# Kernel optimization log

Measured on AMD Instinct MI355X. Metric: run time of the kernel, lower is better.

## Reference

```python
import jax, jax.numpy as jnp
import numpy as np

H, W = 64, 64          # self.shape = (W, H) = (64, 64)
REG_MAX = 16
TOPK = 4

def _dwconv(y, w, b):
    # y: (N, L, C) -> depthwise 3x3 conv on (N, C, H, W) -> (N, L, C)
    N, L, C = y.shape
    img = jnp.transpose(y, (0, 2, 1)).reshape(N, C, H, W)
    out = jax.lax.conv_general_dilated(
        img, w, (1, 1), ((1, 1), (1, 1)),
        dimension_numbers=('NCHW', 'OIHW', 'NCHW'), feature_group_count=C)
    out = out + b[None, :, None, None]
    return jnp.transpose(out.reshape(N, C, H * W), (0, 2, 1))

def _mlp(x, fc1_w, fc1_b, dw1_w, dw1_b, fc2_w, fc2_b, dw2_w, dw2_b, fc3_w, fc3_b):
    h = x @ fc1_w.T + fc1_b
    h = jax.nn.gelu(_dwconv(h, dw1_w, dw1_b), approximate=False)  # torch nn.GELU is exact erf
    h = h @ fc2_w.T + fc2_b
    h = jax.nn.gelu(_dwconv(h, dw2_w, dw2_b), approximate=False)
    return h @ fc3_w.T + fc3_b

def setup_inputs() -> dict:
    key = jax.random.key(0)
    ks = iter(jax.random.split(key, 16))
    d = {}
    d['x'] = jax.random.normal(next(ks), (1, 32, H * W, 256), dtype=jnp.float32)
    for p in ('c_', 'r_'):
        out3 = 1 if p == 'c_' else 4 * (REG_MAX + 1)
        d[p + 'fc1_w'] = 0.02 * jax.random.normal(next(ks), (256, 256), dtype=jnp.float32)
        d[p + 'fc1_b'] = jnp.zeros((256,), jnp.float32)
        d[p + 'dw1_w'] = 0.3 * jax.random.normal(next(ks), (256, 1, 3, 3), dtype=jnp.float32)
        d[p + 'dw1_b'] = jnp.zeros((256,), jnp.float32)
        d[p + 'fc2_w'] = 0.02 * jax.random.normal(next(ks), (256, 256), dtype=jnp.float32)
        d[p + 'fc2_b'] = jnp.zeros((256,), jnp.float32)
        d[p + 'dw2_w'] = 0.3 * jax.random.normal(next(ks), (256, 1, 3, 3), dtype=jnp.float32)
        d[p + 'dw2_b'] = jnp.zeros((256,), jnp.float32)
        d[p + 'fc3_w'] = 0.02 * jax.random.normal(next(ks), (out3, 256), dtype=jnp.float32)
        d[p + 'fc3_b'] = jnp.zeros((out3,), jnp.float32)
    d['rc1_w'] = 0.1 * jax.random.normal(next(ks), (64, 4 * (TOPK + 1)), dtype=jnp.float32)
    d['rc1_b'] = jnp.zeros((64,), jnp.float32)
    d['rc2_w'] = 0.1 * jax.random.normal(next(ks), (1, 64), dtype=jnp.float32)
    d['rc2_b'] = jnp.zeros((1,), jnp.float32)
    return d

def reference(x,
              c_fc1_w, c_fc1_b, c_dw1_w, c_dw1_b, c_fc2_w, c_fc2_b, c_dw2_w, c_dw2_b, c_fc3_w, c_fc3_b,
              r_fc1_w, r_fc1_b, r_dw1_w, r_dw1_b, r_fc2_w, r_fc2_b, r_dw2_w, r_dw2_b, r_fc3_w, r_fc3_b,
              rc1_w, rc1_b, rc2_w, rc2_b):
    xs = x[0]                                   # (N, L, C)
    N = xs.shape[0]
    reg_pred = _mlp(xs, r_fc1_w, r_fc1_b, r_dw1_w, r_dw1_b, r_fc2_w, r_fc2_b,
                    r_dw2_w, r_dw2_b, r_fc3_w, r_fc3_b)  # (N, L, 4*(reg_max+1))
    prob = jax.nn.softmax(
        jnp.transpose(reg_pred, (0, 2, 1)).reshape(N, 4, REG_MAX + 1, H, W), axis=2)
    pt = jnp.transpose(prob, (0, 1, 3, 4, 2))   # (N,4,H,W,reg_max+1)
    topk, _ = jax.lax.top_k(pt, TOPK)           # (N,4,H,W,topk), sorted desc like torch
    stat = jnp.concatenate([topk, topk.mean(axis=-1, keepdims=True)], axis=-1)
    stat = jnp.transpose(stat, (0, 1, 4, 2, 3)).reshape(N, 4 * (TOPK + 1), H, W)
    q = jax.nn.relu(jnp.einsum('nchw,oc->nohw', stat, rc1_w) + rc1_b[None, :, None, None])
    q = jax.nn.sigmoid(jnp.einsum('nchw,oc->nohw', q, rc2_w) + rc2_b[None, :, None, None])
    cls = _mlp(xs, c_fc1_w, c_fc1_b, c_dw1_w, c_dw1_b, c_fc2_w, c_fc2_b,
               c_dw2_w, c_dw2_b, c_fc3_w, c_fc3_b)      # (N, L, 1)
    cls = jax.nn.sigmoid(jnp.transpose(cls, (0, 2, 1)).reshape(N, 1, H, W)) * q
    proj = jnp.arange(REG_MAX + 1, dtype=reg_pred.dtype)  # linspace(0, reg_max, reg_max+1)
    dist = jax.nn.softmax(reg_pred.reshape(-1, REG_MAX + 1), axis=1) @ proj
    boxes = dist.reshape(N, H, W, 4) / REG_MAX
    return cls, boxes, reg_pred.reshape(N, H, W, 4 * (REG_MAX + 1))
```

## Files before the change

### kernel.cpp

```cpp
#include <hip/hip_runtime.h>
#include <hip/hip_bf16.h>

typedef __bf16 bf16x8 __attribute__((ext_vector_type(8)));
typedef float f32x4 __attribute__((ext_vector_type(4)));
typedef float f32x2 __attribute__((ext_vector_type(2)));

__device__ __forceinline__ float bf2f(unsigned short b) {
  unsigned int u = ((unsigned int)b) << 16;
  return __builtin_bit_cast(float, u);
}
__device__ __forceinline__ unsigned short f2bf(float f) {
  unsigned int u = __builtin_bit_cast(unsigned int, f);
  unsigned int r = u + 0x7fffu + ((u >> 16) & 1u);
  return (unsigned short)(r >> 16);
}
__device__ __forceinline__ f32x2 unpack2(unsigned int u) {
  f32x2 r;
  r.x = __builtin_bit_cast(float, u << 16);
  r.y = __builtin_bit_cast(float, u & 0xffff0000u);
  return r;
}

__device__ __forceinline__ void gload16(const void* g, void* l) {
  typedef __attribute__((address_space(1))) const void* gp_t;
  typedef __attribute__((address_space(3))) void* lp_t;
  __builtin_amdgcn_global_load_lds((gp_t)g, (lp_t)l, 16, 0, 0);
}

__device__ __forceinline__ f32x2 gelu2(f32x2 x) {
  f32x2 m = x * x;
  f32x2 t = m * (-0.10295273f) + (-2.3021967f);
  f32x2 u = x * t;
  f32x2 e;
  e.x = __builtin_amdgcn_exp2f(u.x);
  e.y = __builtin_amdgcn_exp2f(u.y);
  f32x2 d = e + 1.0f;
  f32x2 r;
  r.x = __builtin_amdgcn_rcpf(d.x);
  r.y = __builtin_amdgcn_rcpf(d.y);
  return x * r;
}
__device__ __forceinline__ unsigned int cvt_pk_bf16(float lo, float hi) {
  unsigned int r;
  asm("v_cvt_pk_bf16_f32 %0, %1, %2" : "=v"(r) : "v"(lo), "v"(hi));
  return r;
}

__global__ __launch_bounds__(256) void prep_all(
    const float* __restrict__ c1w, const float* __restrict__ r1w,
    const float* __restrict__ c2w, const float* __restrict__ r2w,
    const float* __restrict__ c3w, const float* __restrict__ r3w, const float* __restrict__ r3b,
    const float* __restrict__ c1b, const float* __restrict__ r1b,
    const float* __restrict__ c2b, const float* __restrict__ r2b,
    const float* __restrict__ d1wc, const float* __restrict__ d1bc,
    const float* __restrict__ d1wr, const float* __restrict__ d1br,
    const float* __restrict__ d2wc, const float* __restrict__ d2bc,
    const float* __restrict__ d2wr, const float* __restrict__ d2br,
    unsigned short* __restrict__ w1cat, unsigned short* __restrict__ w2cat,
    unsigned short* __restrict__ c3wb, unsigned short* __restrict__ wr3pad,
    float* __restrict__ br3pad, float* __restrict__ b1cat, float* __restrict__ b2cat,
    float* __restrict__ wd1, float* __restrict__ bd1,
    float* __restrict__ wd2, float* __restrict__ bd2) {
  int i = blockIdx.x * 256 + threadIdx.x;
  {
    int which = i >> 16, j = i & 65535;
    float v = (which == 0) ? c1w[j] : (which == 1) ? r1w[j] : (which == 2) ? c2w[j] : r2w[j];
    unsigned short* dst = (which < 2) ? (w1cat + which * 65536) : (w2cat + (which - 2) * 65536);
    dst[j] = f2bf(v);
  }
  if (i < 32768) {
    int r = i >> 8, c = i & 255;
    wr3pad[i] = (r < 68) ? f2bf(r3w[r * 256 + c]) : (unsigned short)0;
    if (i < 128) br3pad[i] = (i < 68) ? r3b[i] : 0.f;
  }
  if (i < 256) c3wb[i] = f2bf(c3w[i]);
  if (i < 4608) {
    int tap = i >> 9, ch = i & 511, cc = ch & 255;
    wd1[i] = (ch < 256) ? d1wc[cc * 9 + tap] : d1wr[cc * 9 + tap];
    wd2[i] = (ch < 256) ? d2wc[cc * 9 + tap] : d2wr[cc * 9 + tap];
  }
  if (i < 512) {
    bd1[i] = (i < 256) ? d1bc[i] : d1br[i & 255];
    bd2[i] = (i < 256) ? d2bc[i] : d2br[i & 255];
    b1cat[i] = (i < 256) ? c1b[i] : r1b[i & 255];
    b2cat[i] = (i < 256) ? c2b[i] : r2b[i & 255];
  }
}

__global__ __launch_bounds__(256, 2) void gemm_f32a(
    const float* __restrict__ X,
    const unsigned short* __restrict__ W,
    const float* __restrict__ bias,
    unsigned short* __restrict__ Out, int ldo, int lnN) {
  __shared__ unsigned short ldsA[32768];
  __shared__ unsigned short ldsB[2][4096];
  const int nwg = gridDim.x;
  const int bid = blockIdx.x;
  const int wg = (bid & 7) * (nwg >> 3) + (bid >> 3);
  const int mtile = wg >> lnN;
  const int ntile = wg & ((1 << lnN) - 1);
  const long row0 = (long)mtile * 128;
  const int col0 = ntile * 128;

  const int tid = threadIdx.x;
  const int lane = tid & 63;
  const int wid = tid >> 6;
  const int wr = (wid >> 1) * 64;
  const int wc = (wid & 1) * 64;
  const int rr = lane & 15;
  const int gk = lane >> 4;
  const int swz = (rr >> 1) & 3;

  const int srow_l = (wid << 4) + (lane >> 2);
  const int sgl = lane & 3;

  #pragma unroll 4
  for (int j = 0; j < 16; j++) {
    const int s = j * 256 + tid;
    const int row = s >> 5;
    const int glog = s & 31;
    const float* src = X + (row0 + row) * 256L + glog * 8;
    const float4 v0 = *(const float4*)(src);
    const float4 v1 = *(const float4*)(src + 4);
    uint4 pk;
    pk.x = cvt_pk_bf16(v0.x, v0.y);
    pk.y = cvt_pk_bf16(v0.z, v0.w);
    pk.z = cvt_pk_bf16(v1.x, v1.y);
    pk.w = cvt_pk_bf16(v1.z, v1.w);
    const int phys = glog ^ (row & 7);
    *(uint4*)&ldsA[(row * 32 + phys) * 8] = pk;
  }

  auto stageB = [&](int buf, int k0) {
    #pragma unroll
    for (int j = 0; j < 2; j++) {
      const int slotbase = j * 256 + (wid << 6);
      const int row = j * 64 + srow_l;
      const int g = sgl ^ ((row >> 1) & 3);
      gload16(W + (long)(col0 + row) * 256 + k0 + g * 8,
              &ldsB[buf][slotbase * 8]);
    }
  };

  f32x4 acc[4][4] = {};
  stageB(0, 0);
  asm volatile("s_waitcnt vmcnt(0) lgkmcnt(0)" ::: "memory");
  __builtin_amdgcn_s_barrier();

  #pragma unroll
  for (int ks = 0; ks < 8; ks++) {
    if (ks < 7) {
      stageB((ks + 1) & 1, (ks + 1) * 32);
      asm volatile("s_waitcnt vmcnt(2)" ::: "memory");
    } else {
      asm volatile("s_waitcnt vmcnt(0)" ::: "memory");
    }
    __builtin_amdgcn_s_barrier();
    asm volatile("" ::: "memory");
    const unsigned short* bufB = ldsB[ks & 1];
    bf16x8 af[4], bf[4];
    #pragma unroll
    for (int mi = 0; mi < 4; mi++) {
      const int arow = wr + mi * 16 + rr;
      const int aphys = (ks * 4 + gk) ^ (arow & 7);
      af[mi] = __builtin_bit_cast(bf16x8,
          *(const uint4*)&ldsA[(arow * 32 + aphys) * 8]);
    }
    #pragma unroll
    for (int ni = 0; ni < 4; ni++)
      bf[ni] = __builtin_bit_cast(bf16x8,
          *(const uint4*)&bufB[((wc + ni * 16 + rr) * 4 + (gk ^ swz)) * 8]);
    #pragma unroll
    for (int mi = 0; mi < 4; mi++)
      #pragma unroll
      for (int ni = 0; ni < 4; ni++)
        acc[mi][ni] = __builtin_amdgcn_mfma_f32_16x16x32_bf16(af[mi], bf[ni], acc[mi][ni], 0, 0, 0);
    asm volatile("" ::: "memory");
    __builtin_amdgcn_s_barrier();
  }

  #pragma unroll
  for (int mi = 0; mi < 4; mi++) {
    const int rbase = wr + mi * 16 + (lane >> 4) * 4;
    #pragma unroll
    for (int ni = 0; ni < 4; ni++) {
      const int c_ = wc + ni * 16 + (lane & 15);
      const float bv = bias[col0 + c_];
      #pragma unroll
      for (int r = 0; r < 4; r++) {
        Out[(row0 + rbase + r) * (long)ldo + col0 + c_] = f2bf(acc[mi][ni][r] + bv);
      }
    }
  }
}

__global__ __launch_bounds__(256, 3) void gemm_glds(
    const unsigned short* __restrict__ A, int lda, int zAoff,
    const unsigned short* __restrict__ W, int zWoff,
    const float* __restrict__ bias, int zBoff,
    unsigned short* __restrict__ Out, int ldo, int zOoff, int lnN,
    float* __restrict__ OutF) {
  __shared__ unsigned short lds[2][8192];
  const int z = blockIdx.z;
  const unsigned short* Az = A + (long)z * zAoff;
  const unsigned short* Wz = W + (long)z * zWoff;
  const float* biasz = bias + z * zBoff;
  unsigned short* Outz = Out + (long)z * zOoff;

  const int nwg = gridDim.x;
  const int bid = blockIdx.x;
  const int wg = (bid & 7) * (nwg >> 3) + (bid >> 3);
  const int mtile = wg >> lnN;
  const int ntile = wg & ((1 << lnN) - 1);
  const long row0 = (long)mtile * 128;
  const int col0 = ntile * 128;

  const int tid = threadIdx.x;
  const int lane = tid & 63;
  const int wid = tid >> 6;
  const int wr = (wid >> 1) * 64;
  const int wc = (wid & 1) * 64;
  const int rr = lane & 15;
  const int gk = lane >> 4;
  const int swz = (rr >> 1) & 3;

  const int srow_l = (wid << 4) + (lane >> 2);
  const int sgl = lane & 3;

  f32x4 acc[4][4] = {};

  auto stage = [&](int buf, int k0) {
    #pragma unroll
    for (int j = 0; j < 4; j++) {
      const int slotbase = j * 256 + (wid << 6);
      unsigned short* ldst = &lds[buf][slotbase * 8];
      const int row = (j & 1) * 64 + srow_l;
      const int g = sgl ^ ((row >> 1) & 3);
      const unsigned short* src;
      if (j < 2) src = Az + (row0 + row) * (long)lda + k0 + g * 8;
      else       src = Wz + (long)(col0 + row) * 256 + k0 + g * 8;
      gload16(src, ldst);
    }
  };

  stage(0, 0);
  #pragma unroll
  for (int ks = 0; ks < 8; ks++) {
    if (ks < 7) {
      stage((ks + 1) & 1, (ks + 1) * 32);
      asm volatile("s_waitcnt vmcnt(4)" ::: "memory");
    } else {
      asm volatile("s_waitcnt vmcnt(0)" ::: "memory");
    }
    __builtin_amdgcn_s_barrier();
    asm volatile("" ::: "memory");
    const unsigned short* buf = lds[ks & 1];
    bf16x8 af[4], bf[4];
    #pragma unroll
    for (int mi = 0; mi < 4; mi++)
      af[mi] = __builtin_bit_cast(bf16x8,
          *(const uint4*)&buf[(wr + mi * 16 + rr) * 32 + ((gk ^ swz) * 8)]);
    #pragma unroll
    for (int ni = 0; ni < 4; ni++)
      bf[ni] = __builtin_bit_cast(bf16x8,
          *(const uint4*)&buf[4096 + (wc + ni * 16 + rr) * 32 + ((gk ^ swz) * 8)]);
    #pragma unroll
    for (int mi = 0; mi < 4; mi++)
      #pragma unroll
      for (int ni = 0; ni < 4; ni++)
        acc[mi][ni] = __builtin_amdgcn_mfma_f32_16x16x32_bf16(af[mi], bf[ni], acc[mi][ni], 0, 0, 0);
    asm volatile("" ::: "memory");
    __builtin_amdgcn_s_barrier();
  }

  #pragma unroll
  for (int mi = 0; mi < 4; mi++) {
    const int rbase = wr + mi * 16 + (lane >> 4) * 4;
    #pragma unroll
    for (int ni = 0; ni < 4; ni++) {
      const int c_ = wc + ni * 16 + (lane & 15);
      const float bv = biasz[col0 + c_];
      #pragma unroll
      for (int r = 0; r < 4; r++) {
        const float val = acc[mi][ni][r] + bv;
        Outz[(row0 + rbase + r) * (long)ldo + col0 + c_] = f2bf(val);
        if (OutF != nullptr && c_ < 68)
          OutF[(row0 + rbase + r) * 68L + c_] = val;
      }
    }
  }
}

template <bool CLS>
__global__ __launch_bounds__(256) void dwconv_gelu4(
    const unsigned short* __restrict__ In,
    const float* __restrict__ Wt, const float* __restrict__ Bt,
    unsigned short* __restrict__ Out,
    const unsigned short* __restrict__ Wc3, const float* __restrict__ bc3,
    float* __restrict__ cls_logit) {
  const int t = blockIdx.x * 256 + threadIdx.x;
  const int g = t & 63;
  const int p = t >> 6;
  const int n = p >> 10;
  const int h = (p >> 4) & 63;
  const int w0 = (p & 15) << 2;
  const int cbase = g << 3;
  f32x2 acc[4][4];
  {
    float4 b0 = *(const float4*)(Bt + cbase);
    float4 b1 = *(const float4*)(Bt + cbase + 4);
    f32x2 bb[4];
    bb[0].x = b0.x; bb[0].y = b0.y; bb[1].x = b0.z; bb[1].y = b0.w;
    bb[2].x = b1.x; bb[2].y = b1.y; bb[3].x = b1.z; bb[3].y = b1.w;
    #pragma unroll
    for (int k = 0; k < 4; k++)
      #pragma unroll
      for (int i = 0; i < 4; i++) acc[k][i] = bb[i];
  }
  #pragma unroll
  for (int dy = -1; dy <= 1; dy++) {
    const int hh = h + dy;
    if (hh < 0 || hh > 63) continue;
    const float* wbase = Wt + ((dy + 1) * 3) * 512 + cbase;
    f32x2 wt[3][4];
    #pragma unroll
    for (int j = 0; j < 3; j++) {
      float4 a0 = *(const float4*)(wbase + j * 512);
      float4 a1 = *(const float4*)(wbase + j * 512 + 4);
      wt[j][0].x = a0.x; wt[j][0].y = a0.y; wt[j][1].x = a0.z; wt[j][1].y = a0.w;
      wt[j][2].x = a1.x; wt[j][2].y = a1.y; wt[j][3].x = a1.z; wt[j][3].y = a1.w;
    }
    const long rowtok = (long)(((n << 6) + hh) << 6);
    f32x2 f[6][4];
    #pragma unroll
    for (int d = 0; d < 6; d++) {
      const int col = w0 - 1 + d;
      uint4 v = {0u, 0u, 0u, 0u};
      if (col >= 0 && col < 64)
        v = *(const uint4*)(In + (rowtok + col) * 512 + cbase);
      f[d][0] = unpack2(v.x); f[d][1] = unpack2(v.y);
      f[d][2] = unpack2(v.z); f[d][3] = unpack2(v.w);
    }
    #pragma unroll
    for (int k = 0; k < 4; k++)
      #pragma unroll
      for (int j = 0; j < 3; j++)
        #pragma unroll
        for (int i = 0; i < 4; i++)
          acc[k][i] += f[k + j][i] * wt[j][i];
  }
  f32x2 w3[4];
  if (CLS) {
    const int cc = cbase & 255;
    uint4 wv = *(const uint4*)(Wc3 + cc);
    w3[0] = unpack2(wv.x); w3[1] = unpack2(wv.y);
    w3[2] = unpack2(wv.z); w3[3] = unpack2(wv.w);
  }
  const long mbase = ((long)((n << 6) + h) << 6) + w0;
  float s[4];
  #pragma unroll
  for (int k = 0; k < 4; k++) {
    __align__(16) unsigned int ov[4];
    f32x2 ge[4];
    #pragma unroll
    for (int i = 0; i < 4; i++) {
      ge[i] = gelu2(acc[k][i]);
      ov[i] = cvt_pk_bf16(ge[i].x, ge[i].y);
    }
    if (!CLS || cbase >= 256)
      *(uint4*)(Out + (mbase + k) * 512 + cbase) = *(uint4*)ov;
    if (CLS) {
      f32x2 sp = ge[0] * w3[0] + ge[1] * w3[1] + ge[2] * w3[2] + ge[3] * w3[3];
      s[k] = sp.x + sp.y;
    }
  }
  if (CLS) {
    #pragma unroll
    for (int k = 0; k < 4; k++) {
      #pragma unroll
      for (int m = 16; m >= 1; m >>= 1) s[k] += __shfl_xor(s[k], m);
    }
    if (g == 0) {
      float b = bc3[0];
      float4 o;
      o.x = s[0] + b; o.y = s[1] + b; o.z = s[2] + b; o.w = s[3] + b;
      *(float4*)(cls_logit + mbase) = o;
    }
  }
}

__global__ __launch_bounds__(256) void post_kernel(
    const unsigned short* __restrict__ RP,
    const float* __restrict__ cls_logit,
    const float* __restrict__ rc1_w, const float* __restrict__ rc1_b,
    const float* __restrict__ rc2_w, const float* __restrict__ rc2_b,
    float* __restrict__ out_cls, float* __restrict__ out_boxes) {
  int m = blockIdx.x * 256 + threadIdx.x;
  const unsigned short* rp = RP + (long)m * 128;
  __align__(16) unsigned short raw[72];
  #pragma unroll
  for (int q = 0; q < 9; q++)
    *(uint4*)(raw + q * 8) = *(const uint4*)(rp + q * 8);
  float stat[20];
  float4 boxes;
  #pragma unroll
  for (int s = 0; s < 4; s++) {
    float v[17];
    float mx = -1e30f;
    #pragma unroll
    for (int i = 0; i < 17; i++) {
      v[i] = bf2f(raw[s * 17 + i]);
      mx = fmaxf(mx, v[i]);
    }
    float sum = 0.f;
    #pragma unroll
    for (int i = 0; i < 17; i++) { v[i] = __expf(v[i] - mx); sum += v[i]; }
    float inv = 1.f / sum;
    float dist = 0.f;
    #pragma unroll
    for (int i = 0; i < 17; i++) { v[i] *= inv; dist += v[i] * (float)i; }
    ((float*)&boxes)[s] = dist * 0.0625f;
    float tk[4];
    #pragma unroll
    for (int t = 0; t < 4; t++) {
      float bm = v[0]; int bi = 0;
      #pragma unroll
      for (int i = 1; i < 17; i++) {
        if (v[i] > bm) { bm = v[i]; bi = i; }
      }
      tk[t] = bm;
      #pragma unroll
      for (int i = 0; i < 17; i++)
        if (i == bi) v[i] = -1.f;
    }
    stat[s * 5 + 0] = tk[0]; stat[s * 5 + 1] = tk[1];
    stat[s * 5 + 2] = tk[2]; stat[s * 5 + 3] = tk[3];
    stat[s * 5 + 4] = 0.25f * (tk[0] + tk[1] + tk[2] + tk[3]);
  }
  *(float4*)(out_boxes + (long)m * 4) = boxes;
  float z = 0.f;
  #pragma unroll
  for (int o = 0; o < 64; o++) {
    float q = rc1_b[o];
    #pragma unroll
    for (int c = 0; c < 20; c++) q += rc1_w[o * 20 + c] * stat[c];
    q = fmaxf(q, 0.f);
    z += q * rc2_w[o];
  }
  z += rc2_b[0];
  float q2 = 1.f / (1.f + __expf(-z));
  float cl = 1.f / (1.f + __expf(-cls_logit[m]));
  out_cls[m] = cl * q2;
}

extern "C" void kernel_launch(void* const* d_in, const int* in_sizes, int n_in,
                              void* d_out, int out_size, void* d_ws, size_t ws_size,
                              hipStream_t stream) {
  const float* x       = (const float*)d_in[0];
  const float* c_fc1_w = (const float*)d_in[1];
  const float* c_fc1_b = (const float*)d_in[2];
  const float* c_dw1_w = (const float*)d_in[3];
  const float* c_dw1_b = (const float*)d_in[4];
  const float* c_fc2_w = (const float*)d_in[5];
  const float* c_fc2_b = (const float*)d_in[6];
  const float* c_dw2_w = (const float*)d_in[7];
  const float* c_dw2_b = (const float*)d_in[8];
  const float* c_fc3_w = (const float*)d_in[9];
  const float* c_fc3_b = (const float*)d_in[10];
  const float* r_fc1_w = (const float*)d_in[11];
  const float* r_fc1_b = (const float*)d_in[12];
  const float* r_dw1_w = (const float*)d_in[13];
  const float* r_dw1_b = (const float*)d_in[14];
  const float* r_fc2_w = (const float*)d_in[15];
  const float* r_fc2_b = (const float*)d_in[16];
  const float* r_dw2_w = (const float*)d_in[17];
  const float* r_dw2_b = (const float*)d_in[18];
  const float* r_fc3_w = (const float*)d_in[19];
  const float* r_fc3_b = (const float*)d_in[20];
  const float* rc1_w   = (const float*)d_in[21];
  const float* rc1_b   = (const float*)d_in[22];
  const float* rc2_w   = (const float*)d_in[23];
  const float* rc2_b   = (const float*)d_in[24];

  char* ws = (char*)d_ws;
  unsigned short* Hbuf = (unsigned short*)ws;
  unsigned short* Gbuf = (unsigned short*)(ws + 134217728L);
  unsigned short* RP   = (unsigned short*)(ws + 268435456L);
  float* cls_logit     = (float*)(ws + 301989888L);
  char* wb             = ws + 302514176L;
  unsigned short* w1cat  = (unsigned short*)wb;
  unsigned short* w2cat  = w1cat + 131072;
  unsigned short* c3wb   = w2cat + 131072;
  unsigned short* wr3pad = c3wb + 256;
  float* br3pad = (float*)(wr3pad + 32768);
  float* b1cat  = br3pad + 128;
  float* b2cat  = b1cat + 512;
  float* wd1    = b2cat + 512;
  float* bd1    = wd1 + 4608;
  float* wd2    = bd1 + 512;
  float* bd2    = wd2 + 4608;

  float* out_cls   = (float*)d_out;
  float* out_boxes = out_cls + 131072;
  float* out_reg   = out_boxes + 524288;

  prep_all<<<1024, 256, 0, stream>>>(
      c_fc1_w, r_fc1_w, c_fc2_w, r_fc2_w, c_fc3_w, r_fc3_w, r_fc3_b,
      c_fc1_b, r_fc1_b, c_fc2_b, r_fc2_b,
      c_dw1_w, c_dw1_b, r_dw1_w, r_dw1_b,
      c_dw2_w, c_dw2_b, r_dw2_w, r_dw2_b,
      w1cat, w2cat, c3wb, wr3pad, br3pad, b1cat, b2cat,
      wd1, bd1, wd2, bd2);

  gemm_f32a<<<dim3(4096, 1, 1), 256, 0, stream>>>(
      x, w1cat, b1cat, Hbuf, 512, 2);
  dwconv_gelu4<false><<<8192, 256, 0, stream>>>(Hbuf, wd1, bd1, Gbuf,
                                                nullptr, nullptr, nullptr);
  gemm_glds<<<dim3(2048, 1, 2), 256, 0, stream>>>(
      Gbuf, 512, 256, w2cat, 65536, b2cat, 256, Hbuf, 512, 256, 1, nullptr);
  dwconv_gelu4<true><<<8192, 256, 0, stream>>>(Hbuf, wd2, bd2, Gbuf,
                                               c3wb, c_fc3_b, cls_logit);
  gemm_glds<<<dim3(1024, 1, 1), 256, 0, stream>>>(
      Gbuf + 256, 512, 0, wr3pad, 0, br3pad, 0, RP, 128, 0, 0, out_reg);
  post_kernel<<<512, 256, 0, stream>>>(RP, cls_logit, rc1_w, rc1_b, rc2_w, rc2_b,
                                       out_cls, out_boxes);
}
```

Before: 363.7 us.

## Stream fp32 A tiles via async global-to-LDS loads in first GEMM

```diff
diff --git a/kernel.cpp b/kernel.cpp
--- a/kernel.cpp
+++ b/kernel.cpp
@@ -87,12 +87,12 @@
   }
 }
 
-__global__ __launch_bounds__(256, 2) void gemm_f32a(
+__global__ __launch_bounds__(256, 3) void gemm_xa(
     const float* __restrict__ X,
     const unsigned short* __restrict__ W,
     const float* __restrict__ bias,
     unsigned short* __restrict__ Out, int ldo, int lnN) {
-  __shared__ unsigned short ldsA[32768];
+  __shared__ float ldsA[2][4096];
   __shared__ unsigned short ldsB[2][4096];
   const int nwg = gridDim.x;
   const int bid = blockIdx.x;
@@ -114,23 +114,20 @@
   const int srow_l = (wid << 4) + (lane >> 2);
   const int sgl = lane & 3;
 
-  #pragma unroll 4
-  for (int j = 0; j < 16; j++) {
-    const int s = j * 256 + tid;
-    const int row = s >> 5;
-    const int glog = s & 31;
-    const float* src = X + (row0 + row) * 256L + glog * 8;
-    const float4 v0 = *(const float4*)(src);
-    const float4 v1 = *(const float4*)(src + 4);
-    uint4 pk;
-    pk.x = cvt_pk_bf16(v0.x, v0.y);
-    pk.y = cvt_pk_bf16(v0.z, v0.w);
-    pk.z = cvt_pk_bf16(v1.x, v1.y);
-    pk.w = cvt_pk_bf16(v1.z, v1.w);
-    const int phys = glog ^ (row & 7);
-    *(uint4*)&ldsA[(row * 32 + phys) * 8] = pk;
-  }
-
+  const int sA_base = (wid << 6);
+  const int sA_row_l = lane >> 3;
+  const int sA_gp = lane & 7;
+
+  auto stageA = [&](int buf, int k0) {
+    #pragma unroll
+    for (int j = 0; j < 4; j++) {
+      const int gran_base = j * 256 + sA_base;
+      const int row = (gran_base >> 3) + sA_row_l;
+      const int gl = sA_gp ^ (row & 7);
+      gload16(X + (row0 + row) * 256L + k0 + gl * 4,
+              &ldsA[buf][gran_base * 4]);
+    }
+  };
   auto stageB = [&](int buf, int k0) {
     #pragma unroll
     for (int j = 0; j < 2; j++) {
@@ -143,28 +140,34 @@
   };
 
   f32x4 acc[4][4] = {};
+  stageA(0, 0);
   stageB(0, 0);
-  asm volatile("s_waitcnt vmcnt(0) lgkmcnt(0)" ::: "memory");
-  __builtin_amdgcn_s_barrier();
-
   #pragma unroll
   for (int ks = 0; ks < 8; ks++) {
     if (ks < 7) {
+      stageA((ks + 1) & 1, (ks + 1) * 32);
       stageB((ks + 1) & 1, (ks + 1) * 32);
-      asm volatile("s_waitcnt vmcnt(2)" ::: "memory");
+      asm volatile("s_waitcnt vmcnt(6)" ::: "memory");
     } else {
       asm volatile("s_waitcnt vmcnt(0)" ::: "memory");
     }
     __builtin_amdgcn_s_barrier();
     asm volatile("" ::: "memory");
+    const float* bufA = ldsA[ks & 1];
     const unsigned short* bufB = ldsB[ks & 1];
     bf16x8 af[4], bf[4];
     #pragma unroll
     for (int mi = 0; mi < 4; mi++) {
       const int arow = wr + mi * 16 + rr;
-      const int aphys = (ks * 4 + gk) ^ (arow & 7);
-      af[mi] = __builtin_bit_cast(bf16x8,
-          *(const uint4*)&ldsA[(arow * 32 + aphys) * 8]);
+      const int e = arow & 7;
+      const float4 f0 = *(const float4*)&bufA[(arow * 8 + ((2 * gk) ^ e)) * 4];
+      const float4 f1 = *(const float4*)&bufA[(arow * 8 + ((2 * gk + 1) ^ e)) * 4];
+      uint4 au;
+      au.x = cvt_pk_bf16(f0.x, f0.y);
+      au.y = cvt_pk_bf16(f0.z, f0.w);
+      au.z = cvt_pk_bf16(f1.x, f1.y);
+      au.w = cvt_pk_bf16(f1.z, f1.w);
+      af[mi] = __builtin_bit_cast(bf16x8, au);
     }
     #pragma unroll
     for (int ni = 0; ni < 4; ni++)
@@ -194,7 +197,7 @@
   }
 }
 
-__global__ __launch_bounds__(256, 3) void gemm_glds(
+__global__ __launch_bounds__(256, 4) void gemm_glds(
     const unsigned short* __restrict__ A, int lda, int zAoff,
     const unsigned short* __restrict__ W, int zWoff,
     const float* __restrict__ bias, int zBoff,
@@ -512,7 +515,7 @@
       w1cat, w2cat, c3wb, wr3pad, br3pad, b1cat, b2cat,
       wd1, bd1, wd2, bd2);
 
-  gemm_f32a<<<dim3(4096, 1, 1), 256, 0, stream>>>(
+  gemm_xa<<<dim3(4096, 1, 1), 256, 0, stream>>>(
       x, w1cat, b1cat, Hbuf, 512, 2);
   dwconv_gelu4<false><<<8192, 256, 0, stream>>>(Hbuf, wd1, bd1, Gbuf,
                                                 nullptr, nullptr, nullptr);
```

Result: no change. 361.4 us (-0.6%).
